# Kernel optimization log

Hardware: AMD Instinct MI355X
Metric: run time of the kernel (lower is better)

Reference implementation:

```python
import jax, jax.numpy as jnp
import numpy as np

N_NODES = 50000
N_EDGES = 800000
HID = 128
EDGE_DIM = 4
LAYERS = 4
MAX_Z = 100
NUM_GRAPHS = 512


def setup_inputs() -> dict:
    key = jax.random.key(0)
    ks = jax.random.split(key, 16)
    s = lambda k, shape, fan_in: jax.random.normal(k, shape, jnp.float32) / np.sqrt(fan_in)
    inp = {
        "z": jax.random.randint(ks[0], (N_NODES,), 0, MAX_Z + 1),
        "edge_index": jax.random.randint(ks[1], (2, N_EDGES), 0, N_NODES),
        "edge_attr": jax.random.normal(ks[2], (N_EDGES, EDGE_DIM), jnp.float32),
        "batch": jnp.sort(jax.random.randint(ks[3], (N_NODES,), 0, NUM_GRAPHS)),
        "emb": jax.random.normal(ks[4], (MAX_Z + 1, HID), jnp.float32),
        # stacked per-layer params; Linear stored as [in, out]
        "ew1": s(ks[5], (LAYERS, 2 * HID + EDGE_DIM, HID), 2 * HID + EDGE_DIM),
        "eb1": jnp.zeros((LAYERS, HID), jnp.float32),
        "ew2": s(ks[6], (LAYERS, HID, HID), HID),
        "eb2": jnp.zeros((LAYERS, HID), jnp.float32),
        "nw": s(ks[7], (LAYERS, 2 * HID, HID), 2 * HID),
        "nb": jnp.zeros((LAYERS, HID), jnp.float32),
        "rw1": s(ks[8], (HID, HID), HID),
        "rb1": jnp.zeros((HID,), jnp.float32),
        "rw2": s(ks[9], (HID, 1), HID),
        "rb2": jnp.zeros((1,), jnp.float32),
    }
    return inp


def _forward(z, edge_index, edge_attr, batch,
             emb, ew1, eb1, ew2, eb2, nw, nb, rw1, rb1, rw2, rb2):
    silu = jax.nn.silu
    src, dst = edge_index[0], edge_index[1]
    x = emb[z]  # [N, H]
    for l in range(LAYERS):
        m_in = jnp.concatenate([x[src], x[dst], edge_attr], axis=-1)  # [E, 2H+ed]
        h = silu(m_in @ ew1[l] + eb1[l])
        msg = silu(h @ ew2[l] + eb2[l])  # [E, H]
        agg = jax.ops.segment_sum(msg, dst, num_segments=N_NODES)  # scatter-add
        x = silu(jnp.concatenate([x, agg], axis=-1) @ nw[l] + nb[l])
    # segment mean over graphs
    sums = jax.ops.segment_sum(x, batch, num_segments=NUM_GRAPHS)
    counts = jnp.clip(jax.ops.segment_sum(jnp.ones((x.shape[0],), x.dtype), batch,
                                          num_segments=NUM_GRAPHS), 1.0)[:, None]
    g = sums / counts  # [G, H]
    pred = (silu(g @ rw1 + rb1) @ rw2 + rb2)[:, 0]  # [G]
    return pred


def reference(z, edge_index, edge_attr, batch,
              emb, ew1, eb1, ew2, eb2, nw, nb, rw1, rb1, rw2, rb2):
    return _forward(z, edge_index, edge_attr, batch,
                    emb, ew1, eb1, ew2, eb2, nw, nb, rw1, rb1, rw2, rb2)
```

## Files before the change

kernel.cpp:

```cpp
#include <hip/hip_runtime.h>
#include <math.h>

#define HID  128
#define EDIM 4

typedef unsigned short u16;
typedef u16    us8   __attribute__((ext_vector_type(8)));
typedef __bf16 bf16x8 __attribute__((ext_vector_type(8)));
typedef float  f32x4 __attribute__((ext_vector_type(4)));

__device__ __forceinline__ float silu_f(float v) {
    return v * __builtin_amdgcn_rcpf(1.0f + __expf(-v));
}
__device__ __forceinline__ u16 f2bf(float f) {
    unsigned u = __float_as_uint(f);
    unsigned r = u + 0x7fffu + ((u >> 16) & 1u);
    return (u16)(r >> 16);
}
__device__ __forceinline__ u16 f2bf_fast(float f) {
    return (u16)((__float_as_uint(f) + 0x8000u) >> 16);
}
__device__ __forceinline__ unsigned pack_bf2(float a, float b) {
    return ((__float_as_uint(a) + 0x8000u) >> 16) |
           ((__float_as_uint(b) + 0x8000u) & 0xffff0000u);
}
__device__ __forceinline__ float bf2f(u16 s) {
    return __uint_as_float(((unsigned)s) << 16);
}
__device__ __forceinline__ bf16x8 as_bf(us8 v) {
    return __builtin_bit_cast(bf16x8, v);
}

__device__ __forceinline__ void wfrag_one(const float* __restrict__ w,
        u16* __restrict__ out, int KT, int K, int idx) {
    int lane = idx & 63;
    int f    = (idx >> 6) % (KT * 8);
    int l    = idx / (64 * KT * 8);
    int kt = f >> 3, nt = f & 7;
    int n  = nt * 16 + (lane & 15);
    int k0 = kt * 32 + ((lane >> 4) * 8);
    us8 v;
    #pragma unroll
    for (int j = 0; j < 8; ++j) {
        int k = k0 + j;
        v[j] = (k < K) ? f2bf(w[((size_t)l * K + k) * HID + n]) : (u16)0;
    }
    *(us8*)&out[((size_t)(l * KT * 8 + f) * 64 + lane) * 8] = v;
}

#define T1 (4 * 9 * 8 * 64)
#define T2 (4 * 4 * 8 * 64)
#define T3 (4 * 8 * 8 * 64)

__global__ __launch_bounds__(256) void setup_kernel(
        const float* __restrict__ ew1, const float* __restrict__ ew2,
        const float* __restrict__ nw,
        u16* __restrict__ w1f, u16* __restrict__ w2f, u16* __restrict__ nwf,
        int* __restrict__ cnt, int* __restrict__ cursor,
        float* __restrict__ sums, float* __restrict__ cnts_g, int N, int G) {
    int idx = blockIdx.x * 256 + threadIdx.x;
    if (idx < T1) { wfrag_one(ew1, w1f, 9, 2 * HID + EDIM, idx); return; }
    idx -= T1;
    if (idx < T2) { wfrag_one(ew2, w2f, 4, HID, idx); return; }
    idx -= T2;
    if (idx < T3) { wfrag_one(nw, nwf, 8, 2 * HID, idx); return; }
    idx -= T3;
    if (idx < N) { cnt[idx] = 0; return; }
    idx -= N;
    if (idx < N) { cursor[idx] = 0; return; }
    idx -= N;
    if (idx < G * HID) { sums[idx] = 0.f; return; }
    idx -= G * HID;
    if (idx < G) { cnts_g[idx] = 0.f; return; }
}

__global__ __launch_bounds__(256) void hist_kernel(const int* __restrict__ dst,
        int* __restrict__ cnt, int E) {
    int e = blockIdx.x * 256 + threadIdx.x;
    if (e < E) atomicAdd(&cnt[dst[e]], 1);
}

__global__ __launch_bounds__(1024) void scan_kernel(const int* __restrict__ cnt,
        int* __restrict__ rowptr, int n) {
    __shared__ int s[1024];
    const int t = threadIdx.x;
    const int chunk = (n + 1023) >> 10;
    int lo = t * chunk, hi = lo + chunk;
    if (lo > n) lo = n;
    if (hi > n) hi = n;
    int sum = 0;
    for (int i = lo; i < hi; ++i) sum += cnt[i];
    s[t] = sum;
    __syncthreads();
    for (int off = 1; off < 1024; off <<= 1) {
        int v = (t >= off) ? s[t - off] : 0;
        __syncthreads();
        s[t] += v;
        __syncthreads();
    }
    int run = s[t] - sum;
    for (int i = lo; i < hi; ++i) { rowptr[i] = run; run += cnt[i]; }
    if (t == 1023) rowptr[n] = run;
}

__global__ __launch_bounds__(256) void scatter_kernel(const int* __restrict__ src,
        const int* __restrict__ dst, const float* __restrict__ ea,
        const int* __restrict__ rowptr, int* __restrict__ cursor,
        int* __restrict__ srcS, int* __restrict__ dstS, u16* __restrict__ eaS, int E) {
    int e = blockIdx.x * 256 + threadIdx.x;
    if (e >= E) return;
    int d = dst[e];
    int p = rowptr[d] + atomicAdd(&cursor[d], 1);
    srcS[p] = src[e];
    dstS[p] = d;
    const float* q = &ea[(size_t)e * EDIM];
    ushort4 v;
    v.x = f2bf(q[0]); v.y = f2bf(q[1]); v.z = f2bf(q[2]); v.w = f2bf(q[3]);
    *(ushort4*)&eaS[(size_t)p * 4] = v;
}

__global__ __launch_bounds__(HID) void embed_kernel(const int* __restrict__ z,
        const float* __restrict__ emb, u16* __restrict__ xb,
        float* __restrict__ agg, const int* __restrict__ batch,
        float* __restrict__ counts, int n) {
    int i = blockIdx.x;
    if (i >= n) return;
    int t = threadIdx.x;
    xb[(size_t)i * HID + t] = f2bf(emb[(size_t)z[i] * HID + t]);
    agg[(size_t)i * HID + t] = 0.f;
    if (t == 0) unsafeAtomicAdd(&counts[batch[i]], 1.0f);
}

__global__ __launch_bounds__(512, 8) void edge_mfma(
        const u16* __restrict__ xin, const int* __restrict__ srcS,
        const int* __restrict__ dstS, const u16* __restrict__ eaS,
        const u16* __restrict__ w1f, const float* __restrict__ b1,
        const u16* __restrict__ w2f, const float* __restrict__ b2,
        float* __restrict__ agg, int nE) {
    __shared__ __align__(16) char smem[64 * 296 * 2];
    __shared__ int dsh[64];
    u16*   A = (u16*)smem;
    u16*   H = (u16*)smem;
    float* M = (float*)smem;

    const int t    = threadIdx.x;
    const int e0   = blockIdx.x * 64;
    const int wv   = t >> 6, lane = t & 63;
    const int lrow = lane & 15;
    const int kq   = lane >> 4;
    const int kq8  = kq * 8;
    const int rq   = kq * 4;
    const int h    = wv >> 2;
    const int p    = wv & 3;

    #pragma unroll
    for (int it = 0; it < 4; ++it) {
        int slot = it * 512 + t;
        int row = slot >> 5, ch = slot & 31;
        int e = e0 + row; if (e >= nE) e = nE - 1;
        int node = (ch < 16) ? srcS[e] : dstS[e];
        us8 v = *(const us8*)&xin[(size_t)node * HID + (ch & 15) * 8];
        *(us8*)&A[row * 296 + ch * 8] = v;
    }
    if (t < 64) {
        int e = e0 + t;
        bool valid = e < nE; if (!valid) e = nE - 1;
        dsh[t] = valid ? dstS[e] : -1;
        ushort4 q = *(const ushort4*)&eaS[(size_t)e * 4];
        int base = t * 296 + 256;
        A[base + 0] = q.x; A[base + 1] = q.y; A[base + 2] = q.z; A[base + 3] = q.w;
        #pragma unroll
        for (int j = 4; j < 32; ++j) A[base + j] = 0;
    }
    __syncthreads();

    f32x4 acc[2][2];
    #pragma unroll
    for (int nt = 0; nt < 2; ++nt) {
        f32x4 bv = *(const f32x4*)&b1[(p * 2 + nt) * 16 + rq];
        acc[0][nt] = bv; acc[1][nt] = bv;
    }
    #pragma unroll
    for (int kt = 0; kt < 9; ++kt) {
        bf16x8 w0 = *(const bf16x8*)&w1f[((size_t)(kt * 8 + p * 2 + 0) * 64 + lane) * 8];
        bf16x8 w1 = *(const bf16x8*)&w1f[((size_t)(kt * 8 + p * 2 + 1) * 64 + lane) * 8];
        #pragma unroll
        for (int mt = 0; mt < 2; ++mt) {
            bf16x8 a = *(const bf16x8*)&A[((h * 2 + mt) * 16 + lrow) * 296 + kt * 32 + kq8];
            acc[mt][0] = __builtin_amdgcn_mfma_f32_16x16x32_bf16(w0, a, acc[mt][0], 0, 0, 0);
            acc[mt][1] = __builtin_amdgcn_mfma_f32_16x16x32_bf16(w1, a, acc[mt][1], 0, 0, 0);
        }
    }
    __syncthreads();

    #pragma unroll
    for (int mt = 0; mt < 2; ++mt)
        #pragma unroll
        for (int nt = 0; nt < 2; ++nt) {
            uint2 hv;
            hv.x = pack_bf2(silu_f(acc[mt][nt][0]), silu_f(acc[mt][nt][1]));
            hv.y = pack_bf2(silu_f(acc[mt][nt][2]), silu_f(acc[mt][nt][3]));
            int edge = (h * 2 + mt) * 16 + lrow;
            *(uint2*)&H[edge * 136 + (p * 2 + nt) * 16 + rq] = hv;
        }
    __syncthreads();

    f32x4 acc2[2][2];
    #pragma unroll
    for (int nt = 0; nt < 2; ++nt) {
        f32x4 bv = *(const f32x4*)&b2[(p * 2 + nt) * 16 + rq];
        acc2[0][nt] = bv; acc2[1][nt] = bv;
    }
    #pragma unroll
    for (int kt = 0; kt < 4; ++kt) {
        bf16x8 w0 = *(const bf16x8*)&w2f[((size_t)(kt * 8 + p * 2 + 0) * 64 + lane) * 8];
        bf16x8 w1 = *(const bf16x8*)&w2f[((size_t)(kt * 8 + p * 2 + 1) * 64 + lane) * 8];
        #pragma unroll
        for (int mt = 0; mt < 2; ++mt) {
            bf16x8 a = *(const bf16x8*)&H[((h * 2 + mt) * 16 + lrow) * 136 + kt * 32 + kq8];
            acc2[mt][0] = __builtin_amdgcn_mfma_f32_16x16x32_bf16(w0, a, acc2[mt][0], 0, 0, 0);
            acc2[mt][1] = __builtin_amdgcn_mfma_f32_16x16x32_bf16(w1, a, acc2[mt][1], 0, 0, 0);
        }
    }
    __syncthreads();

    #pragma unroll
    for (int mt = 0; mt < 2; ++mt)
        #pragma unroll
        for (int nt = 0; nt < 2; ++nt) {
            f32x4 mv;
            #pragma unroll
            for (int r = 0; r < 4; ++r) mv[r] = silu_f(acc2[mt][nt][r]);
            int edge = (h * 2 + mt) * 16 + lrow;
            *(f32x4*)&M[edge * 132 + (p * 2 + nt) * 16 + rq] = mv;
        }

    {
        int col = p * 32 + (lane & 31);
        int r0  = h * 32 + (lane >> 5) * 16;
        float run = 0.f;
        int   cur = dsh[r0];
        #pragma unroll 4
        for (int i = 0; i < 16; ++i) {
            int row = r0 + i;
            run += M[row * 132 + col];
            int nxt = (i == 15) ? -2 : dsh[row + 1];
            if (cur != nxt) {
                if (cur >= 0)
                    unsafeAtomicAdd(&agg[(size_t)cur * HID + col], run);
                run = 0.f; cur = nxt;
            }
        }
    }
}

__global__ __launch_bounds__(256) void node_mfma(
        u16* __restrict__ xb, float* __restrict__ agg,
        const u16* __restrict__ nwf, const float* __restrict__ nb,
        const int* __restrict__ batch, float* __restrict__ sums,
        int last, int n) {
    const int t    = threadIdx.x;
    const int i0   = blockIdx.x * 32;
    const int wv   = t >> 6, lane = t & 63;
    const int lrow = lane & 15;
    const int kq   = lane >> 4;
    const int kq8  = kq * 8;
    const int rq   = kq * 4;

    int iN[2];
    #pragma unroll
    for (int mt = 0; mt < 2; ++mt) {
        int i = i0 + mt * 16 + lrow; if (i >= n) i = n - 1;
        iN[mt] = i;
    }

    f32x4 acc[2][2];
    {
        float bias0 = nb[wv * 32 + lrow], bias1 = nb[wv * 32 + 16 + lrow];
        #pragma unroll
        for (int mt = 0; mt < 2; ++mt)
            #pragma unroll
            for (int r = 0; r < 4; ++r) {
                acc[mt][0][r] = bias0; acc[mt][1][r] = bias1;
            }
    }
    #pragma unroll
    for (int kt = 0; kt < 4; ++kt) {
        bf16x8 w0 = *(const bf16x8*)&nwf[((size_t)(kt * 8 + wv * 2 + 0) * 64 + lane) * 8];
        bf16x8 w1 = *(const bf16x8*)&nwf[((size_t)(kt * 8 + wv * 2 + 1) * 64 + lane) * 8];
        #pragma unroll
        for (int mt = 0; mt < 2; ++mt) {
            bf16x8 a = as_bf(*(const us8*)&xb[(size_t)iN[mt] * HID + kt * 32 + kq8]);
            acc[mt][0] = __builtin_amdgcn_mfma_f32_16x16x32_bf16(a, w0, acc[mt][0], 0, 0, 0);
            acc[mt][1] = __builtin_amdgcn_mfma_f32_16x16x32_bf16(a, w1, acc[mt][1], 0, 0, 0);
        }
    }
    #pragma unroll
    for (int kt = 4; kt < 8; ++kt) {
        bf16x8 w0 = *(const bf16x8*)&nwf[((size_t)(kt * 8 + wv * 2 + 0) * 64 + lane) * 8];
        bf16x8 w1 = *(const bf16x8*)&nwf[((size_t)(kt * 8 + wv * 2 + 1) * 64 + lane) * 8];
        #pragma unroll
        for (int mt = 0; mt < 2; ++mt) {
            const float* p = &agg[(size_t)iN[mt] * HID + (kt - 4) * 32 + kq8];
            float4 f0 = *(const float4*)p;
            float4 f1 = *(const float4*)(p + 4);
            us8 av;
            av[0] = f2bf_fast(f0.x); av[1] = f2bf_fast(f0.y);
            av[2] = f2bf_fast(f0.z); av[3] = f2bf_fast(f0.w);
            av[4] = f2bf_fast(f1.x); av[5] = f2bf_fast(f1.y);
            av[6] = f2bf_fast(f1.z); av[7] = f2bf_fast(f1.w);
            bf16x8 a = as_bf(av);
            acc[mt][0] = __builtin_amdgcn_mfma_f32_16x16x32_bf16(a, w0, acc[mt][0], 0, 0, 0);
            acc[mt][1] = __builtin_amdgcn_mfma_f32_16x16x32_bf16(a, w1, acc[mt][1], 0, 0, 0);
        }
    }

    if (!last) {
        __syncthreads();
        const float4 z4 = make_float4(0.f, 0.f, 0.f, 0.f);
        #pragma unroll
        for (int kt = 0; kt < 4; ++kt)
            #pragma unroll
            for (int mt = 0; mt < 2; ++mt) {
                float* p = &agg[(size_t)iN[mt] * HID + kt * 32 + kq8];
                *(float4*)p = z4; *(float4*)(p + 4) = z4;
            }
        #pragma unroll
        for (int mt = 0; mt < 2; ++mt)
            #pragma unroll
            for (int nt2 = 0; nt2 < 2; ++nt2)
                #pragma unroll
                for (int r = 0; r < 4; ++r) {
                    int i = i0 + mt * 16 + rq + r;
                    if (i < n)
                        xb[(size_t)i * HID + wv * 32 + nt2 * 16 + lrow] =
                            f2bf_fast(silu_f(acc[mt][nt2][r]));
                }
    } else {
        #pragma unroll
        for (int mt = 0; mt < 2; ++mt)
            #pragma unroll
            for (int nt2 = 0; nt2 < 2; ++nt2)
                #pragma unroll
                for (int r = 0; r < 4; ++r) {
                    int i = i0 + mt * 16 + rq + r;
                    if (i < n) {
                        int b = batch[i];
                        unsafeAtomicAdd(&sums[(size_t)b * HID + wv * 32 + nt2 * 16 + lrow],
                                        silu_f(acc[mt][nt2][r]));
                    }
                }
    }
}

__global__ __launch_bounds__(HID) void readout_kernel(
        const float* __restrict__ sums, const float* __restrict__ counts,
        const float* __restrict__ rw1, const float* __restrict__ rb1,
        const float* __restrict__ rw2, const float* __restrict__ rb2,
        float* __restrict__ pred) {
    __shared__ float gv[HID];
    __shared__ float hv[HID];
    const int g = blockIdx.x;
    const int t = threadIdx.x;
    float c = counts[g];
    if (c < 1.0f) c = 1.0f;
    gv[t] = sums[(size_t)g * HID + t] / c;
    __syncthreads();
    float acc = rb1[t];
    for (int k4 = 0; k4 < 32; ++k4) {
        float4 mv = *(const float4*)&gv[k4 * 4];
        #pragma unroll
        for (int j = 0; j < 4; ++j)
            acc += ((const float*)&mv)[j] * rw1[(size_t)(k4 * 4 + j) * HID + t];
    }
    hv[t] = silu_f(acc) * rw2[t];
    __syncthreads();
    for (int s = HID / 2; s > 0; s >>= 1) {
        if (t < s) hv[t] += hv[t + s];
        __syncthreads();
    }
    if (t == 0) pred[g] = hv[0] + rb2[0];
}

extern "C" void kernel_launch(void* const* d_in, const int* in_sizes, int n_in,
                              void* d_out, int out_size, void* d_ws, size_t ws_size,
                              hipStream_t stream) {
    const int*   z          = (const int*)d_in[0];
    const int*   edge_index = (const int*)d_in[1];
    const float* edge_attr  = (const float*)d_in[2];
    const int*   batch      = (const int*)d_in[3];
    const float* emb        = (const float*)d_in[4];
    const float* ew1        = (const float*)d_in[5];
    const float* eb1        = (const float*)d_in[6];
    const float* ew2        = (const float*)d_in[7];
    const float* eb2        = (const float*)d_in[8];
    const float* nw         = (const float*)d_in[9];
    const float* nb         = (const float*)d_in[10];
    const float* rw1        = (const float*)d_in[11];
    const float* rb1        = (const float*)d_in[12];
    const float* rw2        = (const float*)d_in[13];
    const float* rb2        = (const float*)d_in[14];
    float* pred = (float*)d_out;

    const int N = in_sizes[0];
    const int E = in_sizes[1] / 2;
    const int G = out_size;
    const int* srcI = edge_index;
    const int* dstI = edge_index + E;

    char* base = (char*)d_ws;
    size_t off = 0;
    auto carve = [&](size_t bytes) -> char* {
        char* p = base + off;
        off = (off + bytes + 255) & ~(size_t)255;
        return p;
    };
    float* agg    = (float*)carve((size_t)N * HID * sizeof(float));
    float* sums   = (float*)carve((size_t)G * HID * sizeof(float));
    float* cnts_g = (float*)carve((size_t)G * sizeof(float));
    u16*   xb     = (u16*)carve((size_t)N * HID * sizeof(u16));
    int*   srcS   = (int*)carve((size_t)(E + 64) * sizeof(int));
    int*   dstS   = (int*)carve((size_t)(E + 64) * sizeof(int));
    u16*   eaS    = (u16*)carve((size_t)(E + 64) * 4 * sizeof(u16));
    int*   rowptr = (int*)carve((size_t)(N + 1) * sizeof(int));
    int*   cursor = (int*)carve((size_t)N * sizeof(int));
    int*   cnt    = (int*)carve((size_t)N * sizeof(int));
    u16*   w1f    = (u16*)carve((size_t)4 * 72 * 512 * sizeof(u16));
    u16*   w2f    = (u16*)carve((size_t)4 * 32 * 512 * sizeof(u16));
    u16*   nwf    = (u16*)carve((size_t)4 * 64 * 512 * sizeof(u16));

    {
        long long total = (long long)T1 + T2 + T3 + 2LL * N + (long long)G * HID + G;
        int blocks = (int)((total + 255) / 256);
        setup_kernel<<<blocks, 256, 0, stream>>>(ew1, ew2, nw, w1f, w2f, nwf,
                                                 cnt, cursor, sums, cnts_g, N, G);
    }

    hist_kernel<<<(E + 255) / 256, 256, 0, stream>>>(dstI, cnt, E);
    scan_kernel<<<1, 1024, 0, stream>>>(cnt, rowptr, N);
    scatter_kernel<<<(E + 255) / 256, 256, 0, stream>>>(
        srcI, dstI, edge_attr, rowptr, cursor, srcS, dstS, eaS, E);

    embed_kernel<<<N, HID, 0, stream>>>(z, emb, xb, agg, batch, cnts_g, N);

    for (int l = 0; l < 4; ++l) {
        edge_mfma<<<(E + 63) / 64, 512, 0, stream>>>(
            xb, srcS, dstS, eaS,
            w1f + (size_t)l * 72 * 512, eb1 + (size_t)l * HID,
            w2f + (size_t)l * 32 * 512, eb2 + (size_t)l * HID,
            agg, E);
        node_mfma<<<(N + 31) / 32, 256, 0, stream>>>(
            xb, agg, nwf + (size_t)l * 64 * 512, nb + (size_t)l * HID,
            batch, sums, (l == 3) ? 1 : 0, N);
    }

    readout_kernel<<<G, HID, 0, stream>>>(sums, cnts_g, rw1, rb1, rw2, rb2, pred);
}
```

Before: 1.125 ms.

## Precompute per-node destination projection to shrink the edge GEMM K dimension

Splits the first edge linear layer so the x[dst] part is computed once per node by a new y_kernel into an fp32 buffer Y. The edge kernel then adds Y[dst] into its accumulator init and only runs the src and edge_attr part (K=160 instead of 288). This cuts the edge MFMA work and the gathered x rows per edge by about half. In exchange it adds an extra kernel per layer and an fp32 gather of Y rows per edge. Shared-memory footprint also shrinks, and the dst-index reads in the scatter loop become vectorized.

After: 1.127 ms. Within noise of the previous version (+0.2%).

```diff
diff --git a/kernel.cpp b/kernel.cpp
--- a/kernel.cpp
+++ b/kernel.cpp
@@ -31,8 +31,9 @@
     return __builtin_bit_cast(bf16x8, v);
 }
 
-__device__ __forceinline__ void wfrag_one(const float* __restrict__ w,
-        u16* __restrict__ out, int KT, int K, int idx) {
+__device__ __forceinline__ void wfrag_gen(const float* __restrict__ w,
+        u16* __restrict__ out, int KT, int Kdata, int Kstride,
+        int split, int jump, int idx) {
     int lane = idx & 63;
     int f    = (idx >> 6) % (KT * 8);
     int l    = idx / (64 * KT * 8);
@@ -43,27 +44,33 @@
     #pragma unroll
     for (int j = 0; j < 8; ++j) {
         int k = k0 + j;
-        v[j] = (k < K) ? f2bf(w[((size_t)l * K + k) * HID + n]) : (u16)0;
+        int row = k + (k >= split ? jump : 0);
+        v[j] = (row < Kdata) ? f2bf(w[((size_t)l * Kstride + row) * HID + n]) : (u16)0;
     }
     *(us8*)&out[((size_t)(l * KT * 8 + f) * 64 + lane) * 8] = v;
 }
 
-#define T1 (4 * 9 * 8 * 64)
-#define T2 (4 * 4 * 8 * 64)
-#define T3 (4 * 8 * 8 * 64)
+#define T1A (4 * 5 * 8 * 64)
+#define T1B (4 * 4 * 8 * 64)
+#define T2  (4 * 4 * 8 * 64)
+#define T3  (4 * 8 * 8 * 64)
 
 __global__ __launch_bounds__(256) void setup_kernel(
         const float* __restrict__ ew1, const float* __restrict__ ew2,
         const float* __restrict__ nw,
-        u16* __restrict__ w1f, u16* __restrict__ w2f, u16* __restrict__ nwf,
+        u16* __restrict__ w1af, u16* __restrict__ w1bf,
+        u16* __restrict__ w2f, u16* __restrict__ nwf,
         int* __restrict__ cnt, int* __restrict__ cursor,
         float* __restrict__ sums, float* __restrict__ cnts_g, int N, int G) {
+    const int BIG = 1 << 30;
     int idx = blockIdx.x * 256 + threadIdx.x;
-    if (idx < T1) { wfrag_one(ew1, w1f, 9, 2 * HID + EDIM, idx); return; }
-    idx -= T1;
-    if (idx < T2) { wfrag_one(ew2, w2f, 4, HID, idx); return; }
+    if (idx < T1A) { wfrag_gen(ew1, w1af, 5, 260, 260, 128, 128, idx); return; }
+    idx -= T1A;
+    if (idx < T1B) { wfrag_gen(ew1, w1bf, 4, 260, 260, 0, 128, idx); return; }
+    idx -= T1B;
+    if (idx < T2) { wfrag_gen(ew2, w2f, 4, 128, 128, BIG, 0, idx); return; }
     idx -= T2;
-    if (idx < T3) { wfrag_one(nw, nwf, 8, 2 * HID, idx); return; }
+    if (idx < T3) { wfrag_gen(nw, nwf, 8, 256, 256, BIG, 0, idx); return; }
     idx -= T3;
     if (idx < N) { cnt[idx] = 0; return; }
     idx -= N;
@@ -131,14 +138,60 @@
     if (t == 0) unsafeAtomicAdd(&counts[batch[i]], 1.0f);
 }
 
+__global__ __launch_bounds__(256) void y_kernel(
+        const u16* __restrict__ xb, const u16* __restrict__ w1bf,
+        float* __restrict__ Y, int n) {
+    const int t    = threadIdx.x;
+    const int i0   = blockIdx.x * 32;
+    const int wv   = t >> 6, lane = t & 63;
+    const int lrow = lane & 15;
+    const int kq   = lane >> 4;
+    const int kq8  = kq * 8;
+
+    int iN[2];
+    #pragma unroll
+    for (int mt = 0; mt < 2; ++mt) {
+        int i = i0 + mt * 16 + lrow; if (i >= n) i = n - 1;
+        iN[mt] = i;
+    }
+    f32x4 acc[2][2];
+    #pragma unroll
+    for (int mt = 0; mt < 2; ++mt)
+        #pragma unroll
+        for (int nt = 0; nt < 2; ++nt)
+            acc[mt][nt] = (f32x4){0.f, 0.f, 0.f, 0.f};
+
+    #pragma unroll
+    for (int kt = 0; kt < 4; ++kt) {
+        bf16x8 w0 = *(const bf16x8*)&w1bf[((size_t)(kt * 8 + wv * 2 + 0) * 64 + lane) * 8];
+        bf16x8 w1 = *(const bf16x8*)&w1bf[((size_t)(kt * 8 + wv * 2 + 1) * 64 + lane) * 8];
+        #pragma unroll
+        for (int mt = 0; mt < 2; ++mt) {
+            bf16x8 a = as_bf(*(const us8*)&xb[(size_t)iN[mt] * HID + kt * 32 + kq8]);
+            acc[mt][0] = __builtin_amdgcn_mfma_f32_16x16x32_bf16(w0, a, acc[mt][0], 0, 0, 0);
+            acc[mt][1] = __builtin_amdgcn_mfma_f32_16x16x32_bf16(w1, a, acc[mt][1], 0, 0, 0);
+        }
+    }
+    #pragma unroll
+    for (int mt = 0; mt < 2; ++mt) {
+        int node = i0 + mt * 16 + lrow;
+        if (node < n) {
+            #pragma unroll
+            for (int nt = 0; nt < 2; ++nt)
+                *(f32x4*)&Y[(size_t)node * HID + (wv * 2 + nt) * 16 + kq * 4] = acc[mt][nt];
+        }
+    }
+}
+
 __global__ __launch_bounds__(512, 8) void edge_mfma(
         const u16* __restrict__ xin, const int* __restrict__ srcS,
         const int* __restrict__ dstS, const u16* __restrict__ eaS,
-        const u16* __restrict__ w1f, const float* __restrict__ b1,
+        const u16* __restrict__ w1af, const float* __restrict__ b1,
         const u16* __restrict__ w2f, const float* __restrict__ b2,
+        const float* __restrict__ Y,
         float* __restrict__ agg, int nE) {
-    __shared__ __align__(16) char smem[64 * 296 * 2];
-    __shared__ int dsh[64];
+    __shared__ __align__(16) char smem[64 * 132 * 4];
+    __shared__ __align__(16) int dsh[64];
     u16*   A = (u16*)smem;
     u16*   H = (u16*)smem;
     float* M = (float*)smem;
@@ -154,39 +207,48 @@
     const int p    = wv & 3;
 
     #pragma unroll
-    for (int it = 0; it < 4; ++it) {
+    for (int it = 0; it < 2; ++it) {
         int slot = it * 512 + t;
-        int row = slot >> 5, ch = slot & 31;
+        int row = slot >> 4, ch = slot & 15;
         int e = e0 + row; if (e >= nE) e = nE - 1;
-        int node = (ch < 16) ? srcS[e] : dstS[e];
-        us8 v = *(const us8*)&xin[(size_t)node * HID + (ch & 15) * 8];
-        *(us8*)&A[row * 296 + ch * 8] = v;
+        int node = srcS[e];
+        us8 v = *(const us8*)&xin[(size_t)node * HID + ch * 8];
+        *(us8*)&A[row * 168 + ch * 8] = v;
     }
     if (t < 64) {
         int e = e0 + t;
         bool valid = e < nE; if (!valid) e = nE - 1;
         dsh[t] = valid ? dstS[e] : -1;
         ushort4 q = *(const ushort4*)&eaS[(size_t)e * 4];
-        int base = t * 296 + 256;
+        int base = t * 168 + 128;
+        us8 z8 = (us8){0, 0, 0, 0, 0, 0, 0, 0};
+        *(us8*)&A[base + 8]  = z8;
+        *(us8*)&A[base + 16] = z8;
+        *(us8*)&A[base + 24] = z8;
         A[base + 0] = q.x; A[base + 1] = q.y; A[base + 2] = q.z; A[base + 3] = q.w;
-        #pragma unroll
-        for (int j = 4; j < 32; ++j) A[base + j] = 0;
+        A[base + 4] = 0;   A[base + 5] = 0;   A[base + 6] = 0;   A[base + 7] = 0;
     }
     __syncthreads();
 
     f32x4 acc[2][2];
     #pragma unroll
-    for (int nt = 0; nt < 2; ++nt) {
-        f32x4 bv = *(const f32x4*)&b1[(p * 2 + nt) * 16 + rq];
-        acc[0][nt] = bv; acc[1][nt] = bv;
-    }
-    #pragma unroll
-    for (int kt = 0; kt < 9; ++kt) {
-        bf16x8 w0 = *(const bf16x8*)&w1f[((size_t)(kt * 8 + p * 2 + 0) * 64 + lane) * 8];
-        bf16x8 w1 = *(const bf16x8*)&w1f[((size_t)(kt * 8 + p * 2 + 1) * 64 + lane) * 8];
+    for (int mt = 0; mt < 2; ++mt) {
+        int edge = (h * 2 + mt) * 16 + lrow;
+        int d = dsh[edge]; if (d < 0) d = 0;
+        #pragma unroll
+        for (int nt = 0; nt < 2; ++nt) {
+            f32x4 bv = *(const f32x4*)&b1[(p * 2 + nt) * 16 + rq];
+            f32x4 yv = *(const f32x4*)&Y[(size_t)d * HID + (p * 2 + nt) * 16 + rq];
+            acc[mt][nt] = bv + yv;
+        }
+    }
+    #pragma unroll
+    for (int kt = 0; kt < 5; ++kt) {
+        bf16x8 w0 = *(const bf16x8*)&w1af[((size_t)(kt * 8 + p * 2 + 0) * 64 + lane) * 8];
+        bf16x8 w1 = *(const bf16x8*)&w1af[((size_t)(kt * 8 + p * 2 + 1) * 64 + lane) * 8];
         #pragma unroll
         for (int mt = 0; mt < 2; ++mt) {
-            bf16x8 a = *(const bf16x8*)&A[((h * 2 + mt) * 16 + lrow) * 296 + kt * 32 + kq8];
+            bf16x8 a = *(const bf16x8*)&A[((h * 2 + mt) * 16 + lrow) * 168 + kt * 32 + kq8];
             acc[mt][0] = __builtin_amdgcn_mfma_f32_16x16x32_bf16(w0, a, acc[mt][0], 0, 0, 0);
             acc[mt][1] = __builtin_amdgcn_mfma_f32_16x16x32_bf16(w1, a, acc[mt][1], 0, 0, 0);
         }
@@ -238,13 +300,18 @@
     {
         int col = p * 32 + (lane & 31);
         int r0  = h * 32 + (lane >> 5) * 16;
+        int4 da = *(const int4*)&dsh[r0];
+        int4 db = *(const int4*)&dsh[r0 + 4];
+        int4 dc = *(const int4*)&dsh[r0 + 8];
+        int4 dd = *(const int4*)&dsh[r0 + 12];
+        int ds_[16] = {da.x, da.y, da.z, da.w, db.x, db.y, db.z, db.w,
+                       dc.x, dc.y, dc.z, dc.w, dd.x, dd.y, dd.z, dd.w};
         float run = 0.f;
-        int   cur = dsh[r0];
-        #pragma unroll 4
+        int   cur = ds_[0];
+        #pragma unroll
         for (int i = 0; i < 16; ++i) {
-            int row = r0 + i;
-            run += M[row * 132 + col];
-            int nxt = (i == 15) ? -2 : dsh[row + 1];
+            run += M[(r0 + i) * 132 + col];
+            int nxt = (i == 15) ? -2 : ds_[i + 1];
             if (cur != nxt) {
                 if (cur >= 0)
                     unsafeAtomicAdd(&agg[(size_t)cur * HID + col], run);
@@ -301,9 +368,9 @@
         bf16x8 w1 = *(const bf16x8*)&nwf[((size_t)(kt * 8 + wv * 2 + 1) * 64 + lane) * 8];
         #pragma unroll
         for (int mt = 0; mt < 2; ++mt) {
-            const float* p = &agg[(size_t)iN[mt] * HID + (kt - 4) * 32 + kq8];
-            float4 f0 = *(const float4*)p;
-            float4 f1 = *(const float4*)(p + 4);
+            const float* pa = &agg[(size_t)iN[mt] * HID + (kt - 4) * 32 + kq8];
+            float4 f0 = *(const float4*)pa;
+            float4 f1 = *(const float4*)(pa + 4);
             us8 av;
             av[0] = f2bf_fast(f0.x); av[1] = f2bf_fast(f0.y);
             av[2] = f2bf_fast(f0.z); av[3] = f2bf_fast(f0.w);
@@ -322,8 +389,8 @@
         for (int kt = 0; kt < 4; ++kt)
             #pragma unroll
             for (int mt = 0; mt < 2; ++mt) {
-                float* p = &agg[(size_t)iN[mt] * HID + kt * 32 + kq8];
-                *(float4*)p = z4; *(float4*)(p + 4) = z4;
+                float* pa = &agg[(size_t)iN[mt] * HID + kt * 32 + kq8];
+                *(float4*)pa = z4; *(float4*)(pa + 4) = z4;
             }
         #pragma unroll
         for (int mt = 0; mt < 2; ++mt)
@@ -419,20 +486,22 @@
     float* sums   = (float*)carve((size_t)G * HID * sizeof(float));
     float* cnts_g = (float*)carve((size_t)G * sizeof(float));
     u16*   xb     = (u16*)carve((size_t)N * HID * sizeof(u16));
+    float* Y      = (float*)carve((size_t)N * HID * sizeof(float));
     int*   srcS   = (int*)carve((size_t)(E + 64) * sizeof(int));
     int*   dstS   = (int*)carve((size_t)(E + 64) * sizeof(int));
     u16*   eaS    = (u16*)carve((size_t)(E + 64) * 4 * sizeof(u16));
     int*   rowptr = (int*)carve((size_t)(N + 1) * sizeof(int));
     int*   cursor = (int*)carve((size_t)N * sizeof(int));
     int*   cnt    = (int*)carve((size_t)N * sizeof(int));
-    u16*   w1f    = (u16*)carve((size_t)4 * 72 * 512 * sizeof(u16));
+    u16*   w1af   = (u16*)carve((size_t)4 * 40 * 512 * sizeof(u16));
+    u16*   w1bf   = (u16*)carve((size_t)4 * 32 * 512 * sizeof(u16));
     u16*   w2f    = (u16*)carve((size_t)4 * 32 * 512 * sizeof(u16));
     u16*   nwf    = (u16*)carve((size_t)4 * 64 * 512 * sizeof(u16));
 
     {
-        long long total = (long long)T1 + T2 + T3 + 2LL * N + (long long)G * HID + G;
+        long long total = (long long)T1A + T1B + T2 + T3 + 2LL * N + (long long)G * HID + G;
         int blocks = (int)((total + 255) / 256);
-        setup_kernel<<<blocks, 256, 0, stream>>>(ew1, ew2, nw, w1f, w2f, nwf,
+        setup_kernel<<<blocks, 256, 0, stream>>>(ew1, ew2, nw, w1af, w1bf, w2f, nwf,
                                                  cnt, cursor, sums, cnts_g, N, G);
     }
 
@@ -444,11 +513,13 @@
     embed_kernel<<<N, HID, 0, stream>>>(z, emb, xb, agg, batch, cnts_g, N);
 
     for (int l = 0; l < 4; ++l) {
+        y_kernel<<<(N + 31) / 32, 256, 0, stream>>>(
+            xb, w1bf + (size_t)l * 32 * 512, Y, N);
         edge_mfma<<<(E + 63) / 64, 512, 0, stream>>>(
             xb, srcS, dstS, eaS,
-            w1f + (size_t)l * 72 * 512, eb1 + (size_t)l * HID,
+            w1af + (size_t)l * 40 * 512, eb1 + (size_t)l * HID,
             w2f + (size_t)l * 32 * 512, eb2 + (size_t)l * HID,
-            agg, E);
+            Y, agg, E);
         node_mfma<<<(N + 31) / 32, 256, 0, stream>>>(
             xb, agg, nwf + (size_t)l * 64 * 512, nb + (size_t)l * HID,
             batch, sums, (l == 3) ? 1 : 0, N);
```
